# Kernel tuning notes

Hardware: AMD Instinct MI355X
Metric: run time of the kernel (lower is better)

## Reference

```python
import jax, jax.numpy as jnp
import numpy as np

B, IN_DIM, OUT_DIM = 16384, 1024, 512
N_CAPS, CAP_DIM = 8, 16


def squash(x, axis=-1):
    # scale = |x|^2 / (1 + |x|^2) ; out = scale * x / sqrt(|x|^2 + 1e-8)
    sq = jnp.sum(x * x, axis=axis, keepdims=True)
    return (sq / (1.0 + sq)) * x / jnp.sqrt(sq + 1e-8)


def setup_inputs() -> dict:
    key = jax.random.key(0)
    k1, k2, k3, k4 = jax.random.split(key, 4)
    x = jax.random.normal(k1, (B, IN_DIM), dtype=jnp.float32)
    # Linear(in_dim, n_caps*cap_dim) params (kaiming-ish scale)
    Wp = jax.random.normal(k2, (IN_DIM, N_CAPS * CAP_DIM), dtype=jnp.float32) / np.sqrt(IN_DIM)
    bp = jax.random.normal(k3, (N_CAPS * CAP_DIM,), dtype=jnp.float32) * 0.01
    # routing transform W: [n_caps, cap_dim, out_dim], init std 0.02 as in torch code
    W = jax.random.normal(k4, (N_CAPS, CAP_DIM, OUT_DIM), dtype=jnp.float32) * 0.02
    return {"x": x, "Wp": Wp, "bp": bp, "W": W, "n_routing": 3}


def reference(x, Wp, bp, W, n_routing):
    batch = x.shape[0]
    primary = x @ Wp + bp                                   # [B, n*d]
    primary = primary.reshape(batch, N_CAPS, CAP_DIM)       # [B, n, d]
    primary = squash(primary, axis=-1)
    u_hat = jnp.einsum('bnd,ndo->bno', primary, W)          # [B, n, o]
    b = jnp.zeros((batch, N_CAPS, 1), dtype=x.dtype)
    v = None
    for i in range(n_routing):
        c = jax.nn.softmax(b, axis=1)                       # [B, n, 1]
        s = jnp.sum(c * u_hat, axis=1)                      # [B, o]
        v = squash(s, axis=-1)                              # [B, o]
        if i < n_routing - 1:
            agreement = jnp.einsum('bno,bo->bn', u_hat, v)  # [B, n]
            b = b + agreement[..., None]
    return v
```

## Files before the change

### kernel.cpp

```cpp
#include <hip/hip_runtime.h>
#include <hip/hip_bf16.h>
#include <math.h>

typedef __attribute__((ext_vector_type(8))) short bf16x8;
typedef __attribute__((ext_vector_type(8))) unsigned short u16x8;
typedef __attribute__((ext_vector_type(4))) float f32x4;
typedef __attribute__((ext_vector_type(16))) float f32x16;

__device__ __forceinline__ unsigned short f2bf(float f) {
  unsigned u = __float_as_uint(f);
  return (unsigned short)((u + 0x7FFFu + ((u >> 16) & 1u)) >> 16);
}
__device__ __forceinline__ float bf2f(unsigned short h) {
  return __uint_as_float(((unsigned)h) << 16);
}
__device__ __forceinline__ void cvt8pk_a(const float* f, u16x8& h, u16x8& l) {
  unsigned* hp = (unsigned*)&h;
  unsigned* lp = (unsigned*)&l;
#pragma unroll
  for (int i = 0; i < 4; ++i) {
    __hip_bfloat162 hb = __float22bfloat162_rn(make_float2(f[2*i], f[2*i+1]));
    unsigned hv = *(unsigned*)&hb;
    hp[i] = hv;
    float r0 = f[2*i]     - __uint_as_float(hv << 16);
    float r1 = f[2*i + 1] - __uint_as_float(hv & 0xFFFF0000u);
    __hip_bfloat162 lb = __float22bfloat162_rn(make_float2(r0, r1));
    lp[i] = *(unsigned*)&lb;
  }
}
__device__ __forceinline__ void cvt8pk(const float4& a, const float4& b,
                                       u16x8& h, u16x8& l) {
  float f[8] = {a.x, a.y, a.z, a.w, b.x, b.y, b.z, b.w};
  cvt8pk_a(f, h, l);
}
__device__ __forceinline__ void cvt8b(const float4& a, const float4& b,
                                      bf16x8& h, bf16x8& l) {
  u16x8 hh, ll;
  cvt8pk(a, b, hh, ll);
  h = *(bf16x8*)&hh;
  l = *(bf16x8*)&ll;
}

#define GLD16(g, l) __builtin_amdgcn_global_load_lds( \
    (const __attribute__((address_space(1))) void*)(g), \
    (__attribute__((address_space(3))) void*)(l), 16, 0, 0)

#define MFMA32(a, b, c) __builtin_amdgcn_mfma_f32_32x32x16_bf16(a, b, c, 0, 0, 0)

__global__ __launch_bounds__(256) void caps_prep_all(
    const float* __restrict__ Wp, const float* __restrict__ W,
    unsigned short* __restrict__ th1, unsigned short* __restrict__ tl1,
    unsigned short* __restrict__ th2, unsigned short* __restrict__ tl2,
    unsigned short* __restrict__ th3, unsigned short* __restrict__ tl3)
{
  __shared__ float tile[64][128];
  const int t = threadIdx.x, b = blockIdx.x;
  if (b < 16) {
    const float* src = Wp + (size_t)b * 64 * 128;
#pragma unroll
    for (int i = 0; i < 8; ++i) {
      int j = t + i * 256;
      int kk = j >> 5, q = j & 31;
      *(float4*)&tile[kk][q * 4] = *(const float4*)(src + kk * 128 + q * 4);
    }
    __syncthreads();
    const int col = t >> 1, kg0 = (t & 1) * 4;
    unsigned short hi[32], lo[32];
#pragma unroll
    for (int kk = 0; kk < 32; ++kk) {
      float v = tile[kg0 * 8 + kk][col];
      unsigned short h = f2bf(v);
      hi[kk] = h;
      lo[kk] = f2bf(v - bf2f(h));
    }
#pragma unroll
    for (int i = 0; i < 4; ++i) {
      size_t off = (size_t)b * 8192 + (size_t)(kg0 + i) * 1024 + (size_t)col * 8;
      u16x8 vh, vl;
#pragma unroll
      for (int e = 0; e < 8; ++e) { vh[e] = hi[i * 8 + e]; vl[e] = lo[i * 8 + e]; }
      *(u16x8*)(th1 + off) = vh;
      *(u16x8*)(tl1 + off) = vl;
    }
  } else if (b < 32) {
    int tt = (b - 16) * 256 + t;
#pragma unroll
    for (int h = 0; h < 2; ++h) {
      int c = tt + h * 4096;
      int kt = c >> 12, rem = c & 4095;
      int kg = rem >> 9, col = rem & 511;
      int kbase = kt * 64 + kg * 8;
      u16x8 vh, vl;
#pragma unroll
      for (int e = 0; e < 8; ++e) {
        float v = W[(size_t)(kbase + e) * 512 + col];
        unsigned short hh = f2bf(v);
        vh[e] = hh;
        vl[e] = f2bf(v - bf2f(hh));
      }
      size_t off = ((size_t)(kt * 8 + kg) * 512 + col) * 8;
      *(u16x8*)(th2 + off) = vh;
      *(u16x8*)(tl2 + off) = vl;
    }
  } else {
    int bb = b - 32;
    int a = (bb >> 3) * 16 + (t >> 4);
    int c = (bb & 7) * 16 + (t & 15);
    const float* wa = W + (size_t)a * 512;
    const float* wb = W + (size_t)c * 512;
    float acc = 0.f;
#pragma unroll 4
    for (int o = 0; o < 512; o += 4) {
      float4 xx = *(const float4*)(wa + o);
      float4 yy = *(const float4*)(wb + o);
      acc += xx.x * yy.x + xx.y * yy.y + xx.z * yy.z + xx.w * yy.w;
    }
    unsigned short h = f2bf(acc);
    unsigned short l = f2bf(acc - bf2f(h));
    size_t off = ((size_t)(a >> 3) * 128 + c) * 8 + (a & 7);
    th3[off] = h;
    tl3[off] = l;
  }
}

__global__ __launch_bounds__(512) void caps_primary(
    const float* __restrict__ x, const unsigned short* __restrict__ bth,
    const unsigned short* __restrict__ btl, const float* __restrict__ bp,
    float* __restrict__ p_out)
{
  __shared__ unsigned short lds[49152];
  const int tid  = threadIdx.x;
  const int lane = tid & 63;
  const int w    = tid >> 6;
  const int wm   = w >> 2;
  const int wn   = w & 3;
  const int lc   = lane & 31;
  const int hi   = lane >> 5;
  const int row0 = blockIdx.x * 64;

  const int colB = wn * 32 + lc;
  const int rowA = tid & 63;
  const int kgA0 = tid >> 6;
  const float* xrow = x + (size_t)(row0 + rowA) * 1024;

  f32x16 acc;
#pragma unroll
  for (int j = 0; j < 16; ++j) acc[j] = 0.f;

#pragma unroll 1
  for (int KT = 0; KT < 8; ++KT) {
    {
      const unsigned short* gh = bth + (size_t)KT * 16384 + (size_t)tid * 8;
      const unsigned short* gl = btl + (size_t)KT * 16384 + (size_t)tid * 8;
#pragma unroll
      for (int c = 0; c < 4; ++c) {
        GLD16(gh + c * 4096, lds + 16384 + (c * 512 + tid) * 8);
        GLD16(gl + c * 4096, lds + 32768 + (c * 512 + tid) * 8);
      }
    }
    {
      const float* xp = xrow + KT * 128;
      float4 a0 = *(const float4*)(xp + kgA0 * 8);
      float4 a1 = *(const float4*)(xp + kgA0 * 8 + 4);
      float4 a2 = *(const float4*)(xp + (kgA0 + 8) * 8);
      float4 a3 = *(const float4*)(xp + (kgA0 + 8) * 8 + 4);
      u16x8 h0, l0, h1, l1;
      cvt8pk(a0, a1, h0, l0);
      cvt8pk(a2, a3, h1, l1);
      *(u16x8*)(lds + (kgA0 * 64 + rowA) * 8) = h0;
      *(u16x8*)(lds + 8192 + (kgA0 * 64 + rowA) * 8) = l0;
      *(u16x8*)(lds + ((kgA0 + 8) * 64 + rowA) * 8) = h1;
      *(u16x8*)(lds + 8192 + ((kgA0 + 8) * 64 + rowA) * 8) = l1;
    }
    __syncthreads();

#pragma unroll
    for (int kk = 0; kk < 8; ++kk) {
      const int ks = kk * 2 + hi;
      bf16x8 ah  = *(const bf16x8*)(lds + (ks * 64 + wm * 32 + lc) * 8);
      bf16x8 al  = *(const bf16x8*)(lds + 8192 + (ks * 64 + wm * 32 + lc) * 8);
      bf16x8 bh  = *(const bf16x8*)(lds + 16384 + (ks * 128 + colB) * 8);
      bf16x8 blo = *(const bf16x8*)(lds + 32768 + (ks * 128 + colB) * 8);
      acc = MFMA32(ah, bh,  acc);
      acc = MFMA32(ah, blo, acc);
      acc = MFMA32(al, bh,  acc);
    }
    __syncthreads();
  }

  const float bpv = bp[colB];
#pragma unroll
  for (int r = 0; r < 16; ++r) {
    const int row = wm * 32 + (r & 3) + 8 * (r >> 2) + 4 * hi;
    float val = acc[r] + bpv;
    float sq = val * val;
    sq += __shfl_xor(sq, 1); sq += __shfl_xor(sq, 2);
    sq += __shfl_xor(sq, 4); sq += __shfl_xor(sq, 8);
    float sc = (sq / (1.f + sq)) / sqrtf(sq + 1e-8f);
    p_out[(size_t)(row0 + row) * 128 + colB] = val * sc;
  }
}

__global__ __launch_bounds__(512) void caps_route_g(
    const float* __restrict__ p_in, const unsigned short* __restrict__ mh,
    const unsigned short* __restrict__ ml, float* __restrict__ cs_out)
{
  __shared__ float pT[128 * 65];
  __shared__ unsigned short Msh[32768];
  __shared__ float t_lds[64 * 9];
  __shared__ float c_lds[64 * 9];
  const int tid  = threadIdx.x;
  const int lane = tid & 63;
  const int w    = tid >> 6;
  const int wm   = w >> 2;
  const int wn   = w & 3;
  const int lc   = lane & 31;
  const int hi   = lane >> 5;
  const int row0 = blockIdx.x * 64;

#pragma unroll
  for (int i = 0; i < 4; ++i) {
    int idx = tid + i * 512;
    *(u16x8*)&Msh[idx * 8] = *(const u16x8*)(mh + (size_t)idx * 8);
    *(u16x8*)&Msh[16384 + idx * 8] = *(const u16x8*)(ml + (size_t)idx * 8);
  }
#pragma unroll
  for (int i = 0; i < 4; ++i) {
    int j = tid + i * 512;
    int r = j >> 5, c4 = j & 31;
    f32x4 v = *(const f32x4*)(p_in + (size_t)(row0 + r) * 128 + c4 * 4);
    pT[(c4 * 4 + 0) * 65 + r] = v[0];
    pT[(c4 * 4 + 1) * 65 + r] = v[1];
    pT[(c4 * 4 + 2) * 65 + r] = v[2];
    pT[(c4 * 4 + 3) * 65 + r] = v[3];
  }
  if (w == 0) {
#pragma unroll
    for (int n = 0; n < 8; ++n) c_lds[lane * 9 + n] = 0.125f;
  }
  __syncthreads();

  const int arow = wm * 32 + lc;
  const int col  = wn * 32 + lc;
  const int cap  = wn * 2 + (lc >> 4);
  float bb[8] = {0.f, 0.f, 0.f, 0.f, 0.f, 0.f, 0.f, 0.f};

#pragma unroll 1
  for (int it = 0; it < 3; ++it) {
    f32x16 acc;
#pragma unroll
    for (int j = 0; j < 16; ++j) acc[j] = 0.f;

#pragma unroll
    for (int kk = 0; kk < 8; ++kk) {
      const float cv = c_lds[arow * 9 + kk];
      float q[8];
#pragma unroll
      for (int e = 0; e < 8; ++e)
        q[e] = pT[(kk * 16 + hi * 8 + e) * 65 + arow] * cv;
      u16x8 hq, lq;
      cvt8pk_a(q, hq, lq);
      const int fi = ((kk * 2 + hi) * 128 + col) * 8;
      bf16x8 mbh = *(const bf16x8*)&Msh[fi];
      bf16x8 mbl = *(const bf16x8*)&Msh[16384 + fi];
      acc = MFMA32(*(bf16x8*)&hq, mbh, acc);
      acc = MFMA32(*(bf16x8*)&hq, mbl, acc);
      acc = MFMA32(*(bf16x8*)&lq, mbh, acc);
    }

    float tp[16];
#pragma unroll
    for (int r = 0; r < 16; ++r) {
      const int row = wm * 32 + (r & 3) + 8 * (r >> 2) + 4 * hi;
      float prod = pT[col * 65 + row] * acc[r];
      prod += __shfl_xor(prod, 1);
      prod += __shfl_xor(prod, 2);
      prod += __shfl_xor(prod, 4);
      prod += __shfl_xor(prod, 8);
      tp[r] = prod;
    }
    __syncthreads();
    if ((lc & 15) == 0) {
#pragma unroll
      for (int r = 0; r < 16; ++r) {
        const int row = wm * 32 + (r & 3) + 8 * (r >> 2) + 4 * hi;
        t_lds[row * 9 + cap] = tp[r];
      }
    }
    __syncthreads();

    if (w == 0) {
      float c[8], t[8];
#pragma unroll
      for (int n = 0; n < 8; ++n) {
        c[n] = c_lds[lane * 9 + n];
        t[n] = t_lds[lane * 9 + n];
      }
      float ss = 0.f;
#pragma unroll
      for (int n = 0; n < 8; ++n) ss = fmaf(c[n], t[n], ss);
      float scale = (ss / (1.f + ss)) / sqrtf(ss + 1e-8f);
      if (it < 2) {
#pragma unroll
        for (int n = 0; n < 8; ++n) bb[n] += scale * t[n];
        float mx = bb[0];
#pragma unroll
        for (int n = 1; n < 8; ++n) mx = fmaxf(mx, bb[n]);
        float e[8], Z = 0.f;
#pragma unroll
        for (int n = 0; n < 8; ++n) { e[n] = expf(bb[n] - mx); Z += e[n]; }
        float inv = 1.f / Z;
#pragma unroll
        for (int n = 0; n < 8; ++n) c_lds[lane * 9 + n] = e[n] * inv;
      } else {
        f32x4 c0 = {scale * c[0], scale * c[1], scale * c[2], scale * c[3]};
        f32x4 c1 = {scale * c[4], scale * c[5], scale * c[6], scale * c[7]};
        *(f32x4*)(cs_out + (size_t)(row0 + lane) * 8)     = c0;
        *(f32x4*)(cs_out + (size_t)(row0 + lane) * 8 + 4) = c1;
      }
    }
    __syncthreads();
  }
}

__global__ __launch_bounds__(512) void caps_vout(
    const float* __restrict__ p, const unsigned short* __restrict__ bth,
    const unsigned short* __restrict__ btl, const float* __restrict__ cs,
    float* __restrict__ out)
{
  __shared__ unsigned short Bsh[32768];
  const int tid  = threadIdx.x;
  const int lane = tid & 63;
  const int w    = tid >> 6;
  const int wm   = w >> 2;
  const int wn   = w & 3;
  const int lc   = lane & 31;
  const int hi   = lane >> 5;
  const int row0 = blockIdx.x * 64;
  const int col0 = blockIdx.y * 128;

#pragma unroll
  for (int i = 0; i < 4; ++i) {
    int idx = tid + i * 512;
    int kt = idx >> 10, kg = (idx >> 7) & 7, col = idx & 127;
    size_t g = ((size_t)(kt * 8 + kg) * 512 + col0 + col) * 8;
    *(u16x8*)&Bsh[idx * 8] = *(const u16x8*)(bth + g);
    *(u16x8*)&Bsh[16384 + idx * 8] = *(const u16x8*)(btl + g);
  }

  const int rA = row0 + wm * 32 + lc;
  const float* qp = p + (size_t)rA * 128;
  float cs8[8];
  *(f32x4*)&cs8[0] = *(const f32x4*)(cs + (size_t)rA * 8);
  *(f32x4*)&cs8[4] = *(const f32x4*)(cs + (size_t)rA * 8 + 4);
  __syncthreads();

  f32x16 acc;
#pragma unroll
  for (int j = 0; j < 16; ++j) acc[j] = 0.f;

#pragma unroll
  for (int kt = 0; kt < 2; ++kt) {
#pragma unroll
    for (int kk = 0; kk < 4; ++kk) {
      const float* qk = qp + kt * 64 + kk * 16 + hi * 8;
      float4 a0 = *(const float4*)(qk);
      float4 a1 = *(const float4*)(qk + 4);
      const float cv = cs8[kt * 4 + kk];
      a0.x *= cv; a0.y *= cv; a0.z *= cv; a0.w *= cv;
      a1.x *= cv; a1.y *= cv; a1.z *= cv; a1.w *= cv;
      bf16x8 ah, al;
      cvt8b(a0, a1, ah, al);
      const int ks = kk * 2 + hi;
      const int fi = ((kt * 8 + ks) * 128 + wn * 32 + lc) * 8;
      bf16x8 bh  = *(const bf16x8*)&Bsh[fi];
      bf16x8 blo = *(const bf16x8*)&Bsh[16384 + fi];
      acc = MFMA32(ah, bh,  acc);
      acc = MFMA32(ah, blo, acc);
      acc = MFMA32(al, bh,  acc);
    }
  }

#pragma unroll
  for (int r = 0; r < 16; ++r) {
    const int row = (r & 3) + 8 * (r >> 2) + 4 * hi;
    out[(size_t)(row0 + wm * 32 + row) * 512 + col0 + wn * 32 + lc] = acc[r];
  }
}

extern "C" void kernel_launch(void* const* d_in, const int* in_sizes, int n_in,
                              void* d_out, int out_size, void* d_ws, size_t ws_size,
                              hipStream_t stream) {
  (void)in_sizes; (void)n_in; (void)out_size; (void)ws_size;
  const float* x  = (const float*)d_in[0];
  const float* Wp = (const float*)d_in[1];
  const float* bp = (const float*)d_in[2];
  const float* W  = (const float*)d_in[3];
  char* ws = (char*)d_ws;
  float* p_ws = (float*)ws;
  unsigned short* th1 = (unsigned short*)(ws + 8388608);
  unsigned short* tl1 = (unsigned short*)(ws + 8650752);
  unsigned short* th2 = (unsigned short*)(ws + 8912896);
  unsigned short* tl2 = (unsigned short*)(ws + 9043968);
  unsigned short* th3 = (unsigned short*)(ws + 9175040);
  unsigned short* tl3 = (unsigned short*)(ws + 9207808);
  float* cs_ws = (float*)(ws + 9240576);
  float* outp = (float*)d_out;

  caps_prep_all<<<96, 256, 0, stream>>>(Wp, W, th1, tl1, th2, tl2, th3, tl3);
  caps_primary<<<256, 512, 0, stream>>>(x, th1, tl1, bp, p_ws);
  caps_route_g<<<256, 512, 0, stream>>>(p_ws, th3, tl3, cs_ws);
  caps_vout<<<dim3(256, 4), 512, 0, stream>>>(p_ws, th2, tl2, cs_ws, outp);
}
```

Baseline: 90.43 us.

## Fuse routing-coefficient stage into primary capsule kernel and stage x as fp32 via direct loads

Merges the routing kernel into the primary-capsule GEMM kernel, so the squashed primary capsules go straight into LDS as a transposed tile instead of being re-read from global memory by a second launch. The routing matrix M is now read from global memory (through the cache) instead of being staged into LDS. The x tile is also loaded into LDS as raw fp32 with async global-to-LDS loads, and the bf16 hi/lo split now happens at MFMA operand load time. This removes one kernel launch and one round trip of the intermediate, at the cost of repeated split conversions per wave and global-latency reads of M inside the routing loop.

Result: no change. 91.59 us (+1.3%).

```diff
diff --git a/kernel.cpp b/kernel.cpp
--- a/kernel.cpp
+++ b/kernel.cpp
@@ -126,7 +126,8 @@
 __global__ __launch_bounds__(512) void caps_primary(
     const float* __restrict__ x, const unsigned short* __restrict__ bth,
     const unsigned short* __restrict__ btl, const float* __restrict__ bp,
-    float* __restrict__ p_out)
+    const unsigned short* __restrict__ mh, const unsigned short* __restrict__ ml,
+    float* __restrict__ p_out, float* __restrict__ cs_out)
 {
   __shared__ unsigned short lds[49152];
   const int tid  = threadIdx.x;
@@ -139,9 +140,7 @@
   const int row0 = blockIdx.x * 64;
 
   const int colB = wn * 32 + lc;
-  const int rowA = tid & 63;
-  const int kgA0 = tid >> 6;
-  const float* xrow = x + (size_t)(row0 + rowA) * 1024;
+  const int arow = wm * 32 + lc;
 
   f32x16 acc;
 #pragma unroll
@@ -149,6 +148,13 @@
 
 #pragma unroll 1
   for (int KT = 0; KT < 8; ++KT) {
+#pragma unroll
+    for (int i = 0; i < 4; ++i) {
+      int c = tid + i * 512;
+      const float* gx = x + (size_t)(row0 + (c & 63)) * 1024
+                        + KT * 128 + (c >> 7) * 8 + ((c >> 6) & 1) * 4;
+      GLD16(gx, lds + c * 8);
+    }
     {
       const unsigned short* gh = bth + (size_t)KT * 16384 + (size_t)tid * 8;
       const unsigned short* gl = btl + (size_t)KT * 16384 + (size_t)tid * 8;
@@ -158,36 +164,29 @@
         GLD16(gl + c * 4096, lds + 32768 + (c * 512 + tid) * 8);
       }
     }
-    {
-      const float* xp = xrow + KT * 128;
-      float4 a0 = *(const float4*)(xp + kgA0 * 8);
-      float4 a1 = *(const float4*)(xp + kgA0 * 8 + 4);
-      float4 a2 = *(const float4*)(xp + (kgA0 + 8) * 8);
-      float4 a3 = *(const float4*)(xp + (kgA0 + 8) * 8 + 4);
-      u16x8 h0, l0, h1, l1;
-      cvt8pk(a0, a1, h0, l0);
-      cvt8pk(a2, a3, h1, l1);
-      *(u16x8*)(lds + (kgA0 * 64 + rowA) * 8) = h0;
-      *(u16x8*)(lds + 8192 + (kgA0 * 64 + rowA) * 8) = l0;
-      *(u16x8*)(lds + ((kgA0 + 8) * 64 + rowA) * 8) = h1;
-      *(u16x8*)(lds + 8192 + ((kgA0 + 8) * 64 + rowA) * 8) = l1;
-    }
-    __syncthreads();
-
+    __syncthreads();
+
+    const float* Af = (const float*)lds;
 #pragma unroll
     for (int kk = 0; kk < 8; ++kk) {
       const int ks = kk * 2 + hi;
-      bf16x8 ah  = *(const bf16x8*)(lds + (ks * 64 + wm * 32 + lc) * 8);
-      bf16x8 al  = *(const bf16x8*)(lds + 8192 + (ks * 64 + wm * 32 + lc) * 8);
+      f32x4 a0 = *(const f32x4*)&Af[((ks * 2 + 0) * 64 + arow) * 4];
+      f32x4 a1 = *(const f32x4*)&Af[((ks * 2 + 1) * 64 + arow) * 4];
+      float f[8] = {a0[0], a0[1], a0[2], a0[3], a1[0], a1[1], a1[2], a1[3]};
+      u16x8 hq, lq;
+      cvt8pk_a(f, hq, lq);
       bf16x8 bh  = *(const bf16x8*)(lds + 16384 + (ks * 128 + colB) * 8);
       bf16x8 blo = *(const bf16x8*)(lds + 32768 + (ks * 128 + colB) * 8);
-      acc = MFMA32(ah, bh,  acc);
-      acc = MFMA32(ah, blo, acc);
-      acc = MFMA32(al, bh,  acc);
-    }
-    __syncthreads();
-  }
-
+      acc = MFMA32(*(bf16x8*)&hq, bh,  acc);
+      acc = MFMA32(*(bf16x8*)&hq, blo, acc);
+      acc = MFMA32(*(bf16x8*)&lq, bh,  acc);
+    }
+    __syncthreads();
+  }
+
+  float* pT     = (float*)lds;
+  float* t_lds  = (float*)lds + 8320;
+  float* c_lds  = (float*)lds + 8896;
   const float bpv = bp[colB];
 #pragma unroll
   for (int r = 0; r < 16; ++r) {
@@ -197,42 +196,9 @@
     sq += __shfl_xor(sq, 1); sq += __shfl_xor(sq, 2);
     sq += __shfl_xor(sq, 4); sq += __shfl_xor(sq, 8);
     float sc = (sq / (1.f + sq)) / sqrtf(sq + 1e-8f);
-    p_out[(size_t)(row0 + row) * 128 + colB] = val * sc;
-  }
-}
-
-__global__ __launch_bounds__(512) void caps_route_g(
-    const float* __restrict__ p_in, const unsigned short* __restrict__ mh,
-    const unsigned short* __restrict__ ml, float* __restrict__ cs_out)
-{
-  __shared__ float pT[128 * 65];
-  __shared__ unsigned short Msh[32768];
-  __shared__ float t_lds[64 * 9];
-  __shared__ float c_lds[64 * 9];
-  const int tid  = threadIdx.x;
-  const int lane = tid & 63;
-  const int w    = tid >> 6;
-  const int wm   = w >> 2;
-  const int wn   = w & 3;
-  const int lc   = lane & 31;
-  const int hi   = lane >> 5;
-  const int row0 = blockIdx.x * 64;
-
-#pragma unroll
-  for (int i = 0; i < 4; ++i) {
-    int idx = tid + i * 512;
-    *(u16x8*)&Msh[idx * 8] = *(const u16x8*)(mh + (size_t)idx * 8);
-    *(u16x8*)&Msh[16384 + idx * 8] = *(const u16x8*)(ml + (size_t)idx * 8);
-  }
-#pragma unroll
-  for (int i = 0; i < 4; ++i) {
-    int j = tid + i * 512;
-    int r = j >> 5, c4 = j & 31;
-    f32x4 v = *(const f32x4*)(p_in + (size_t)(row0 + r) * 128 + c4 * 4);
-    pT[(c4 * 4 + 0) * 65 + r] = v[0];
-    pT[(c4 * 4 + 1) * 65 + r] = v[1];
-    pT[(c4 * 4 + 2) * 65 + r] = v[2];
-    pT[(c4 * 4 + 3) * 65 + r] = v[3];
+    float pv = val * sc;
+    p_out[(size_t)(row0 + row) * 128 + colB] = pv;
+    pT[colB * 65 + row] = pv;
   }
   if (w == 0) {
 #pragma unroll
@@ -240,16 +206,14 @@
   }
   __syncthreads();
 
-  const int arow = wm * 32 + lc;
-  const int col  = wn * 32 + lc;
-  const int cap  = wn * 2 + (lc >> 4);
+  const int cap = wn * 2 + (lc >> 4);
   float bb[8] = {0.f, 0.f, 0.f, 0.f, 0.f, 0.f, 0.f, 0.f};
 
 #pragma unroll 1
   for (int it = 0; it < 3; ++it) {
-    f32x16 acc;
-#pragma unroll
-    for (int j = 0; j < 16; ++j) acc[j] = 0.f;
+    f32x16 racc;
+#pragma unroll
+    for (int j = 0; j < 16; ++j) racc[j] = 0.f;
 
 #pragma unroll
     for (int kk = 0; kk < 8; ++kk) {
@@ -260,19 +224,19 @@
         q[e] = pT[(kk * 16 + hi * 8 + e) * 65 + arow] * cv;
       u16x8 hq, lq;
       cvt8pk_a(q, hq, lq);
-      const int fi = ((kk * 2 + hi) * 128 + col) * 8;
-      bf16x8 mbh = *(const bf16x8*)&Msh[fi];
-      bf16x8 mbl = *(const bf16x8*)&Msh[16384 + fi];
-      acc = MFMA32(*(bf16x8*)&hq, mbh, acc);
-      acc = MFMA32(*(bf16x8*)&hq, mbl, acc);
-      acc = MFMA32(*(bf16x8*)&lq, mbh, acc);
+      const int fi = ((kk * 2 + hi) * 128 + colB) * 8;
+      bf16x8 mbh = *(const bf16x8*)(mh + fi);
+      bf16x8 mbl = *(const bf16x8*)(ml + fi);
+      racc = MFMA32(*(bf16x8*)&hq, mbh, racc);
+      racc = MFMA32(*(bf16x8*)&hq, mbl, racc);
+      racc = MFMA32(*(bf16x8*)&lq, mbh, racc);
     }
 
     float tp[16];
 #pragma unroll
     for (int r = 0; r < 16; ++r) {
       const int row = wm * 32 + (r & 3) + 8 * (r >> 2) + 4 * hi;
-      float prod = pT[col * 65 + row] * acc[r];
+      float prod = pT[colB * 65 + row] * racc[r];
       prod += __shfl_xor(prod, 1);
       prod += __shfl_xor(prod, 2);
       prod += __shfl_xor(prod, 4);
@@ -408,7 +372,6 @@
   float* outp = (float*)d_out;
 
   caps_prep_all<<<96, 256, 0, stream>>>(Wp, W, th1, tl1, th2, tl2, th3, tl3);
-  caps_primary<<<256, 512, 0, stream>>>(x, th1, tl1, bp, p_ws);
-  caps_route_g<<<256, 512, 0, stream>>>(p_ws, th3, tl3, cs_ws);
+  caps_primary<<<256, 512, 0, stream>>>(x, th1, tl1, bp, th3, tl3, p_ws, cs_ws);
   caps_vout<<<dim3(256, 4), 512, 0, stream>>>(p_ws, th2, tl2, cs_ws, outp);
 }
```
